# Kernel tuning notes

Measured on AMD Instinct MI355X. Metric: run time of the kernel, lower is better.

The kernel has to match this reference:

```python
import jax, jax.numpy as jnp
import numpy as np

BRANCH_PROB = 0.3
BRANCH_THRESHOLD = 0.6
DECAY_VISITED_FACTOR = 0.02
LR_DECAY = 0.001
LR_PATH = 0.02
NOISE_STD = 0.05
SPARK_ENERGY_DECAY = 0.98
SPARK_FORCE_STEPS = 5

N = 8192
S = 256  # max concurrent sparks (vectorized with an active mask)


def setup_inputs() -> dict:
    key = jax.random.key(0)
    ks = jax.random.split(key, 10)
    W = 0.1 * jax.random.normal(ks[0], (N, N), dtype=jnp.float32)
    s = jax.random.uniform(ks[1], (N,), dtype=jnp.float32)
    visited = jax.random.bernoulli(ks[2], 0.05, (N, N))
    noise = jax.random.normal(ks[3], (N,), dtype=jnp.float32)
    spark_pos = jax.random.randint(ks[4], (S,), 0, N)
    spark_energy = 0.05 + 0.95 * jax.random.uniform(ks[5], (S,), dtype=jnp.float32)
    spark_age = jax.random.randint(ks[6], (S,), 0, 10)
    spark_active = jax.random.bernoulli(ks[7], 0.9, (S,))
    u_main = jax.random.uniform(ks[8], (S,), dtype=jnp.float32)
    u_branch = jax.random.uniform(ks[9], (S, N), dtype=jnp.float32)
    return {"W": W, "s": s, "visited": visited, "noise": noise,
            "spark_pos": spark_pos, "spark_energy": spark_energy,
            "spark_age": spark_age, "spark_active": spark_active,
            "u_main": u_main, "u_branch": u_branch}


def reference(W, s, visited, noise, spark_pos, spark_energy, spark_age,
              spark_active, u_main, u_branch):
    n = W.shape[0]
    # global state update: s = sigmoid(W @ (0.95*s) + noise)
    s = jax.nn.sigmoid(W @ (0.95 * s) + NOISE_STD * noise)

    # force young active sparks' positions to 1.0
    force = spark_active & (spark_age < SPARK_FORCE_STEPS)
    force_cnt = jnp.zeros((n,), jnp.int32).at[spark_pos].add(force.astype(jnp.int32))
    s = jnp.where(force_cnt > 0, jnp.asarray(1.0, s.dtype), s)

    # per-spark transition distribution from pre-update W rows
    rows = W[spark_pos]                                   # [S, n]
    positive = jax.nn.relu(rows) + 1e-6
    probs = positive / positive.sum(-1, keepdims=True)
    cdf = jnp.cumsum(probs, axis=-1)
    main_next = jnp.minimum((cdf < u_main[:, None]).sum(-1), n - 1)   # inverse-CDF multinomial
    main_onehot = jax.nn.one_hot(main_next, n, dtype=W.dtype)
    # branch to every strong candidate independently with prob BRANCH_PROB
    branch = ((positive > BRANCH_THRESHOLD) & (u_branch < BRANCH_PROB)).astype(W.dtype)
    counts = (main_onehot + branch) * spark_active[:, None].astype(W.dtype)  # [S, n] edge multiplicity

    # scatter path-reinforcement updates: W[pos, nxt] += LR_PATH * energy (per traversal)
    W_new = W.at[spark_pos].add(LR_PATH * spark_energy[:, None] * counts)

    # visited edges
    edge_hits = jnp.zeros((n, n), jnp.int8).at[spark_pos].add((counts > 0).astype(jnp.int8))
    visited_new = visited | (edge_hits > 0)

    # masked decay + clamp over full matrix
    decay = jnp.where(visited_new,
                      jnp.asarray(1.0 - LR_DECAY * DECAY_VISITED_FACTOR, W.dtype),
                      jnp.asarray(1.0 - LR_DECAY, W.dtype))
    W_new = jnp.clip(W_new * decay, -2.0, 2.0)
    return W_new, s, visited_new
```

## Files before the change

kernel.cpp:

```cpp
#include <hip/hip_runtime.h>

#define NN 8192
#define SS 256

__device__ __forceinline__ float decay_clamp(float w, bool vis) {
    const float d = vis ? 0.99998f : 0.999f;
    const float x = w * d;
    return fminf(fmaxf(x, -2.0f), 2.0f);
}

__global__ __launch_bounds__(256)
void fusedSpark(const float* __restrict__ W, const float* __restrict__ s,
                const unsigned int* __restrict__ visited, const float* __restrict__ noise,
                const int* __restrict__ spark_pos, const float* __restrict__ energy,
                const int* __restrict__ age, const unsigned int* __restrict__ active,
                const float* __restrict__ u_main, const float* __restrict__ u_branch,
                float* __restrict__ outW, float* __restrict__ outS, float* __restrict__ outV)
{
    const int row  = blockIdx.x;
    const int tid  = threadIdx.x;
    const int lane = tid & 63;
    const int wv   = tid >> 6;
    const size_t rowOff = (size_t)row * NN;

    __shared__ unsigned long long wmask[4];
    __shared__ int   s_force;
    __shared__ float m_add[SS];
    __shared__ int   m_u[SS];
    __shared__ int   m_main[SS];
    __shared__ double part[SS];
    __shared__ int    ired[SS];
    __shared__ float  red[SS];

    const bool match = (active[tid] != 0u) && (spark_pos[tid] == row);
    const unsigned long long bal = __ballot(match);
    if (lane == 0) wmask[wv] = bal;
    if (tid == 0)  s_force = 0;
    __syncthreads();
    if (match && age[tid] < 5) atomicOr(&s_force, 1);
    int nMatch = 0;
#pragma unroll
    for (int w = 0; w < 4; ++w) nMatch += __popcll(wmask[w]);
    if (match) {
        int rank = __popcll(bal & ((1ull << lane) - 1ull));
        for (int w = 0; w < wv; ++w) rank += __popcll(wmask[w]);
        m_add[rank] = 0.02f * energy[tid];
        m_u[rank]   = tid;
    }
    __syncthreads();

    float acc = 0.0f;

    if (nMatch == 0) {
        const float4* __restrict__ W4 = reinterpret_cast<const float4*>(W + rowOff);
        const uint4*  __restrict__ V4 = reinterpret_cast<const uint4*>(visited + rowOff);
        const float4* __restrict__ s4 = reinterpret_cast<const float4*>(s);
        float4* __restrict__ oW = reinterpret_cast<float4*>(outW + rowOff);
        float4* __restrict__ oV = reinterpret_cast<float4*>(outV + rowOff);
#pragma unroll
        for (int i = 0; i < 8; ++i) {
            const int idx = i * 256 + tid;
            const float4 w  = W4[idx];
            const float4 sv = s4[idx];
            acc += w.x * (0.95f * sv.x);
            acc += w.y * (0.95f * sv.y);
            acc += w.z * (0.95f * sv.z);
            acc += w.w * (0.95f * sv.w);
            const uint4 v = V4[idx];
            float4 ow, ov;
            ow.x = decay_clamp(w.x, v.x != 0u); ov.x = (v.x != 0u) ? 1.0f : 0.0f;
            ow.y = decay_clamp(w.y, v.y != 0u); ov.y = (v.y != 0u) ? 1.0f : 0.0f;
            ow.z = decay_clamp(w.z, v.z != 0u); ov.z = (v.z != 0u) ? 1.0f : 0.0f;
            ow.w = decay_clamp(w.w, v.w != 0u); ov.w = (v.w != 0u) ? 1.0f : 0.0f;
            oW[idx] = ow;
            oV[idx] = ov;
        }
    } else {
        const float* __restrict__ Wrow = W + rowOff;
        const int base = tid * 32;
        double lsum = 0.0;
        for (int k = 0; k < 32; ++k) {
            const float wval = Wrow[base + k];
            acc  += wval * (0.95f * s[base + k]);
            lsum += (double)(fmaxf(wval, 0.0f) + 1e-6f);
        }
        part[tid] = lsum;
        __syncthreads();
        for (int off = 1; off < 256; off <<= 1) {
            const double v = (tid >= off) ? part[tid - off] : 0.0;
            __syncthreads();
            part[tid] += v;
            __syncthreads();
        }
        const double total = part[255];
        const double excl  = (tid == 0) ? 0.0 : part[tid - 1];

        for (int m = 0; m < nMatch; ++m) {
            const double thr = (double)u_main[m_u[m]] * total;
            double run = excl;
            int cnt = 0;
            for (int k = 0; k < 32; ++k) {
                run += (double)(fmaxf(Wrow[base + k], 0.0f) + 1e-6f);
                cnt += (run < thr) ? 1 : 0;
            }
            ired[tid] = cnt;
            __syncthreads();
            for (int off = 128; off > 0; off >>= 1) {
                if (tid < off) ired[tid] += ired[tid + off];
                __syncthreads();
            }
            if (tid == 0) m_main[m] = min(ired[0], NN - 1);
            __syncthreads();
        }

        const float4* __restrict__ W4 = reinterpret_cast<const float4*>(W + rowOff);
        const uint4*  __restrict__ V4 = reinterpret_cast<const uint4*>(visited + rowOff);
        float4* __restrict__ oW = reinterpret_cast<float4*>(outW + rowOff);
        float4* __restrict__ oV = reinterpret_cast<float4*>(outV + rowOff);
        for (int i = 0; i < 8; ++i) {
            const int idx = i * 256 + tid;
            const float4 w = W4[idx];
            const uint4  v = V4[idx];
            const float wf[4] = {w.x, w.y, w.z, w.w};
            const unsigned int vf[4] = {v.x, v.y, v.z, v.w};
            float ow[4], ov[4];
            const int jb = idx * 4;
#pragma unroll
            for (int c = 0; c < 4; ++c) {
                const int j = jb + c;
                const float wval = wf[c];
                const float pvv  = fmaxf(wval, 0.0f) + 1e-6f;
                float wt  = wval;
                bool  hit = false;
                for (int k = 0; k < nMatch; ++k) {
                    float cts = 0.0f;
                    if (j == m_main[k]) cts += 1.0f;
                    if (pvv > 0.6f) {
                        if (u_branch[(size_t)m_u[k] * NN + j] < 0.3f) cts += 1.0f;
                    }
                    if (cts != 0.0f) { hit = true; wt += m_add[k] * cts; }
                }
                const bool vis = (vf[c] != 0u) || hit;
                ow[c] = decay_clamp(wt, vis);
                ov[c] = vis ? 1.0f : 0.0f;
            }
            oW[idx] = make_float4(ow[0], ow[1], ow[2], ow[3]);
            oV[idx] = make_float4(ov[0], ov[1], ov[2], ov[3]);
        }
    }

    red[tid] = acc;
    __syncthreads();
    for (int off = 128; off > 0; off >>= 1) {
        if (tid < off) red[tid] += red[tid + off];
        __syncthreads();
    }
    if (tid == 0) {
        const float y = red[0] + 0.05f * noise[row];
        outS[row] = (s_force != 0) ? 1.0f : (1.0f / (1.0f + expf(-y)));
    }
}

extern "C" void kernel_launch(void* const* d_in, const int* in_sizes, int n_in,
                              void* d_out, int out_size, void* d_ws, size_t ws_size,
                              hipStream_t stream) {
    const float*        W         = (const float*)d_in[0];
    const float*        s         = (const float*)d_in[1];
    const unsigned int* visited   = (const unsigned int*)d_in[2];
    const float*        noise     = (const float*)d_in[3];
    const int*          spark_pos = (const int*)d_in[4];
    const float*        energy    = (const float*)d_in[5];
    const int*          age       = (const int*)d_in[6];
    const unsigned int* active    = (const unsigned int*)d_in[7];
    const float*        u_main    = (const float*)d_in[8];
    const float*        u_branch  = (const float*)d_in[9];

    float* outW = (float*)d_out;
    float* outS = outW + (size_t)NN * NN;
    float* outV = outS + NN;

    (void)d_ws; (void)ws_size;

    fusedSpark<<<NN, 256, 0, stream>>>(W, s, visited, noise, spark_pos, energy,
                                       age, active, u_main, u_branch,
                                       outW, outS, outV);
}
```

Measured before the change: 202.3 us.

## Split spark rows into a separate kernel and slim the plain-row kernel

```diff
diff --git a/kernel.cpp b/kernel.cpp
--- a/kernel.cpp
+++ b/kernel.cpp
@@ -3,150 +3,180 @@
 #define NN 8192
 #define SS 256
 
+typedef float        f4  __attribute__((ext_vector_type(4)));
+typedef unsigned int ui4 __attribute__((ext_vector_type(4)));
+
 __device__ __forceinline__ float decay_clamp(float w, bool vis) {
     const float d = vis ? 0.99998f : 0.999f;
-    const float x = w * d;
-    return fminf(fmaxf(x, -2.0f), 2.0f);
+    return fminf(fmaxf(w * d, -2.0f), 2.0f);
+}
+
+__global__ __launch_bounds__(256, 8)
+void fastRows(const float* __restrict__ W, const float* __restrict__ s,
+              const unsigned int* __restrict__ visited, const float* __restrict__ noise,
+              const int* __restrict__ spark_pos, const unsigned int* __restrict__ active,
+              float* __restrict__ outW, float* __restrict__ outS, float* __restrict__ outV)
+{
+    const int row = blockIdx.x;
+    const int tid = threadIdx.x;
+
+    __shared__ int s_has;
+    if (tid == 0) s_has = 0;
+    __syncthreads();
+    const bool match = (active[tid] != 0u) && (spark_pos[tid] == row);
+    if (match) atomicOr(&s_has, 1);
+    __syncthreads();
+    if (s_has) return;
+
+    const size_t rowOff = (size_t)row * NN;
+    const f4*  __restrict__ W4 = reinterpret_cast<const f4*>(W + rowOff);
+    const ui4* __restrict__ V4 = reinterpret_cast<const ui4*>(visited + rowOff);
+    const f4*  __restrict__ s4 = reinterpret_cast<const f4*>(s);
+    f4* __restrict__ oW = reinterpret_cast<f4*>(outW + rowOff);
+    f4* __restrict__ oV = reinterpret_cast<f4*>(outV + rowOff);
+
+    float acc = 0.0f;
+#pragma unroll
+    for (int i = 0; i < 8; ++i) {
+        const int idx = i * 256 + tid;
+        const f4  w  = __builtin_nontemporal_load(W4 + idx);
+        const ui4 v  = __builtin_nontemporal_load(V4 + idx);
+        const f4  sv = s4[idx];
+        acc += w.x * (0.95f * sv.x);
+        acc += w.y * (0.95f * sv.y);
+        acc += w.z * (0.95f * sv.z);
+        acc += w.w * (0.95f * sv.w);
+        f4 ow, ov;
+        ow.x = decay_clamp(w.x, v.x != 0u); ov.x = (v.x != 0u) ? 1.0f : 0.0f;
+        ow.y = decay_clamp(w.y, v.y != 0u); ov.y = (v.y != 0u) ? 1.0f : 0.0f;
+        ow.z = decay_clamp(w.z, v.z != 0u); ov.z = (v.z != 0u) ? 1.0f : 0.0f;
+        ow.w = decay_clamp(w.w, v.w != 0u); ov.w = (v.w != 0u) ? 1.0f : 0.0f;
+        __builtin_nontemporal_store(ow, oW + idx);
+        __builtin_nontemporal_store(ov, oV + idx);
+    }
+
+    for (int off = 32; off > 0; off >>= 1) acc += __shfl_down(acc, off, 64);
+    __shared__ float red[4];
+    if ((tid & 63) == 0) red[tid >> 6] = acc;
+    __syncthreads();
+    if (tid == 0) {
+        const float y = red[0] + red[1] + red[2] + red[3] + 0.05f * noise[row];
+        outS[row] = 1.0f / (1.0f + expf(-y));
+    }
 }
 
 __global__ __launch_bounds__(256)
-void fusedSpark(const float* __restrict__ W, const float* __restrict__ s,
-                const unsigned int* __restrict__ visited, const float* __restrict__ noise,
-                const int* __restrict__ spark_pos, const float* __restrict__ energy,
-                const int* __restrict__ age, const unsigned int* __restrict__ active,
-                const float* __restrict__ u_main, const float* __restrict__ u_branch,
-                float* __restrict__ outW, float* __restrict__ outS, float* __restrict__ outV)
+void sparkRows(const float* __restrict__ W, const float* __restrict__ s,
+               const unsigned int* __restrict__ visited, const float* __restrict__ noise,
+               const int* __restrict__ spark_pos, const float* __restrict__ energy,
+               const int* __restrict__ age, const unsigned int* __restrict__ active,
+               const float* __restrict__ u_main, const float* __restrict__ u_branch,
+               float* __restrict__ outW, float* __restrict__ outS, float* __restrict__ outV)
 {
-    const int row  = blockIdx.x;
-    const int tid  = threadIdx.x;
-    const int lane = tid & 63;
-    const int wv   = tid >> 6;
+    const int sp = blockIdx.x;
+    if (active[sp] == 0u) return;
+    const int row = spark_pos[sp];
+    for (int t = 0; t < sp; ++t)
+        if (active[t] != 0u && spark_pos[t] == row) return;
+    const int tid = threadIdx.x;
     const size_t rowOff = (size_t)row * NN;
 
-    __shared__ unsigned long long wmask[4];
-    __shared__ int   s_force;
-    __shared__ float m_add[SS];
-    __shared__ int   m_u[SS];
-    __shared__ int   m_main[SS];
+    __shared__ float  m_add[SS];
+    __shared__ int    m_u[SS];
+    __shared__ int    m_main[SS];
+    __shared__ int    s_cnt, s_force;
     __shared__ double part[SS];
     __shared__ int    ired[SS];
     __shared__ float  red[SS];
 
-    const bool match = (active[tid] != 0u) && (spark_pos[tid] == row);
-    const unsigned long long bal = __ballot(match);
-    if (lane == 0) wmask[wv] = bal;
-    if (tid == 0)  s_force = 0;
-    __syncthreads();
-    if (match && age[tid] < 5) atomicOr(&s_force, 1);
-    int nMatch = 0;
-#pragma unroll
-    for (int w = 0; w < 4; ++w) nMatch += __popcll(wmask[w]);
-    if (match) {
-        int rank = __popcll(bal & ((1ull << lane) - 1ull));
-        for (int w = 0; w < wv; ++w) rank += __popcll(wmask[w]);
-        m_add[rank] = 0.02f * energy[tid];
-        m_u[rank]   = tid;
-    }
-    __syncthreads();
-
-    float acc = 0.0f;
-
-    if (nMatch == 0) {
-        const float4* __restrict__ W4 = reinterpret_cast<const float4*>(W + rowOff);
-        const uint4*  __restrict__ V4 = reinterpret_cast<const uint4*>(visited + rowOff);
-        const float4* __restrict__ s4 = reinterpret_cast<const float4*>(s);
-        float4* __restrict__ oW = reinterpret_cast<float4*>(outW + rowOff);
-        float4* __restrict__ oV = reinterpret_cast<float4*>(outV + rowOff);
-#pragma unroll
-        for (int i = 0; i < 8; ++i) {
-            const int idx = i * 256 + tid;
-            const float4 w  = W4[idx];
-            const float4 sv = s4[idx];
-            acc += w.x * (0.95f * sv.x);
-            acc += w.y * (0.95f * sv.y);
-            acc += w.z * (0.95f * sv.z);
-            acc += w.w * (0.95f * sv.w);
-            const uint4 v = V4[idx];
-            float4 ow, ov;
-            ow.x = decay_clamp(w.x, v.x != 0u); ov.x = (v.x != 0u) ? 1.0f : 0.0f;
-            ow.y = decay_clamp(w.y, v.y != 0u); ov.y = (v.y != 0u) ? 1.0f : 0.0f;
-            ow.z = decay_clamp(w.z, v.z != 0u); ov.z = (v.z != 0u) ? 1.0f : 0.0f;
-            ow.w = decay_clamp(w.w, v.w != 0u); ov.w = (v.w != 0u) ? 1.0f : 0.0f;
-            oW[idx] = ow;
-            oV[idx] = ov;
+    if (tid == 0) {
+        int c = 0, f = 0;
+        for (int u = sp; u < SS; ++u)
+            if (active[u] != 0u && spark_pos[u] == row) {
+                m_add[c] = 0.02f * energy[u];
+                m_u[c]   = u;
+                if (age[u] < 5) f = 1;
+                ++c;
+            }
+        s_cnt = c; s_force = f;
+    }
+    __syncthreads();
+    const int nMatch = s_cnt;
+
+    const float* __restrict__ Wrow = W + rowOff;
+    const int base = tid * 32;
+    float  acc  = 0.0f;
+    double lsum = 0.0;
+    for (int k = 0; k < 32; ++k) {
+        const float wval = Wrow[base + k];
+        acc  += wval * (0.95f * s[base + k]);
+        lsum += (double)(fmaxf(wval, 0.0f) + 1e-6f);
+    }
+    part[tid] = lsum;
+    __syncthreads();
+    for (int off = 1; off < 256; off <<= 1) {
+        const double v = (tid >= off) ? part[tid - off] : 0.0;
+        __syncthreads();
+        part[tid] += v;
+        __syncthreads();
+    }
+    const double total = part[255];
+    const double excl  = (tid == 0) ? 0.0 : part[tid - 1];
+
+    for (int m = 0; m < nMatch; ++m) {
+        const double thr = (double)u_main[m_u[m]] * total;
+        double run = excl;
+        int cnt = 0;
+        for (int k = 0; k < 32; ++k) {
+            run += (double)(fmaxf(Wrow[base + k], 0.0f) + 1e-6f);
+            cnt += (run < thr) ? 1 : 0;
         }
-    } else {
-        const float* __restrict__ Wrow = W + rowOff;
-        const int base = tid * 32;
-        double lsum = 0.0;
-        for (int k = 0; k < 32; ++k) {
-            const float wval = Wrow[base + k];
-            acc  += wval * (0.95f * s[base + k]);
-            lsum += (double)(fmaxf(wval, 0.0f) + 1e-6f);
-        }
-        part[tid] = lsum;
-        __syncthreads();
-        for (int off = 1; off < 256; off <<= 1) {
-            const double v = (tid >= off) ? part[tid - off] : 0.0;
-            __syncthreads();
-            part[tid] += v;
+        ired[tid] = cnt;
+        __syncthreads();
+        for (int off = 128; off > 0; off >>= 1) {
+            if (tid < off) ired[tid] += ired[tid + off];
             __syncthreads();
         }
-        const double total = part[255];
-        const double excl  = (tid == 0) ? 0.0 : part[tid - 1];
-
-        for (int m = 0; m < nMatch; ++m) {
-            const double thr = (double)u_main[m_u[m]] * total;
-            double run = excl;
-            int cnt = 0;
-            for (int k = 0; k < 32; ++k) {
-                run += (double)(fmaxf(Wrow[base + k], 0.0f) + 1e-6f);
-                cnt += (run < thr) ? 1 : 0;
+        if (tid == 0) m_main[m] = min(ired[0], NN - 1);
+        __syncthreads();
+    }
+
+    const f4*  __restrict__ W4 = reinterpret_cast<const f4*>(W + rowOff);
+    const ui4* __restrict__ V4 = reinterpret_cast<const ui4*>(visited + rowOff);
+    f4* __restrict__ oW = reinterpret_cast<f4*>(outW + rowOff);
+    f4* __restrict__ oV = reinterpret_cast<f4*>(outV + rowOff);
+    for (int i = 0; i < 8; ++i) {
+        const int idx = i * 256 + tid;
+        const f4  w = W4[idx];
+        const ui4 v = V4[idx];
+        const float wf[4] = {w.x, w.y, w.z, w.w};
+        const unsigned int vf[4] = {v.x, v.y, v.z, v.w};
+        float ow[4], ov[4];
+        const int jb = idx * 4;
+#pragma unroll
+        for (int c = 0; c < 4; ++c) {
+            const int j = jb + c;
+            const float wval = wf[c];
+            const float pvv  = fmaxf(wval, 0.0f) + 1e-6f;
+            float wt  = wval;
+            bool  hit = false;
+            for (int k = 0; k < nMatch; ++k) {
+                float cts = 0.0f;
+                if (j == m_main[k]) cts += 1.0f;
+                if (pvv > 0.6f) {
+                    if (u_branch[(size_t)m_u[k] * NN + j] < 0.3f) cts += 1.0f;
+                }
+                if (cts != 0.0f) { hit = true; wt += m_add[k] * cts; }
             }
-            ired[tid] = cnt;
-            __syncthreads();
-            for (int off = 128; off > 0; off >>= 1) {
-                if (tid < off) ired[tid] += ired[tid + off];
-                __syncthreads();
-            }
-            if (tid == 0) m_main[m] = min(ired[0], NN - 1);
-            __syncthreads();
+            const bool vis = (vf[c] != 0u) || hit;
+            ow[c] = decay_clamp(wt, vis);
+            ov[c] = vis ? 1.0f : 0.0f;
         }
-
-        const float4* __restrict__ W4 = reinterpret_cast<const float4*>(W + rowOff);
-        const uint4*  __restrict__ V4 = reinterpret_cast<const uint4*>(visited + rowOff);
-        float4* __restrict__ oW = reinterpret_cast<float4*>(outW + rowOff);
-        float4* __restrict__ oV = reinterpret_cast<float4*>(outV + rowOff);
-        for (int i = 0; i < 8; ++i) {
-            const int idx = i * 256 + tid;
-            const float4 w = W4[idx];
-            const uint4  v = V4[idx];
-            const float wf[4] = {w.x, w.y, w.z, w.w};
-            const unsigned int vf[4] = {v.x, v.y, v.z, v.w};
-            float ow[4], ov[4];
-            const int jb = idx * 4;
-#pragma unroll
-            for (int c = 0; c < 4; ++c) {
-                const int j = jb + c;
-                const float wval = wf[c];
-                const float pvv  = fmaxf(wval, 0.0f) + 1e-6f;
-                float wt  = wval;
-                bool  hit = false;
-                for (int k = 0; k < nMatch; ++k) {
-                    float cts = 0.0f;
-                    if (j == m_main[k]) cts += 1.0f;
-                    if (pvv > 0.6f) {
-                        if (u_branch[(size_t)m_u[k] * NN + j] < 0.3f) cts += 1.0f;
-                    }
-                    if (cts != 0.0f) { hit = true; wt += m_add[k] * cts; }
-                }
-                const bool vis = (vf[c] != 0u) || hit;
-                ow[c] = decay_clamp(wt, vis);
-                ov[c] = vis ? 1.0f : 0.0f;
-            }
-            oW[idx] = make_float4(ow[0], ow[1], ow[2], ow[3]);
-            oV[idx] = make_float4(ov[0], ov[1], ov[2], ov[3]);
-        }
+        f4 owv, ovv;
+        owv.x = ow[0]; owv.y = ow[1]; owv.z = ow[2]; owv.w = ow[3];
+        ovv.x = ov[0]; ovv.y = ov[1]; ovv.z = ov[2]; ovv.w = ov[3];
+        __builtin_nontemporal_store(owv, oW + idx);
+        __builtin_nontemporal_store(ovv, oV + idx);
     }
 
     red[tid] = acc;
@@ -181,7 +211,9 @@
 
     (void)d_ws; (void)ws_size;
 
-    fusedSpark<<<NN, 256, 0, stream>>>(W, s, visited, noise, spark_pos, energy,
-                                       age, active, u_main, u_branch,
-                                       outW, outS, outV);
-}
+    fastRows <<<NN, 256, 0, stream>>>(W, s, visited, noise, spark_pos, active,
+                                      outW, outS, outV);
+    sparkRows<<<SS, 256, 0, stream>>>(W, s, visited, noise, spark_pos, energy,
+                                      age, active, u_main, u_branch,
+                                      outW, outS, outV);
+}
```

Result: slower. 222.7 us (+10.1%).
